# Kernel tuning notes

Measured on AMD Instinct MI355X. Metric: run time of the kernel, lower is better.

Reference implementation:

```python
import jax, jax.numpy as jnp
import numpy as np

EPS = 1e-5

def _ln(x, g, b):
    m = jnp.mean(x, axis=-1, keepdims=True)
    v = jnp.var(x, axis=-1, keepdims=True)
    return (x - m) * jax.lax.rsqrt(v + EPS) * g + b

def _gelu(x):
    return jax.nn.gelu(x, approximate=False)  # torch nn.GELU default is exact erf

def setup_inputs() -> dict:
    key = jax.random.key(0)
    B, N, D, H = 4, 1024, 128, 12
    HID = H * D
    ks = jax.random.split(key, 16)
    s = lambda k, sh, fan: jax.random.normal(k, sh, jnp.float32) * (fan ** -0.5)
    return {
        "x": jax.random.normal(ks[0], (B, N, D), jnp.float32),
        # project: LN(D) -> Linear(D,HID) -> GELU -> Linear(HID,HID)
        "ln1_g": jnp.ones((D,), jnp.float32), "ln1_b": jnp.zeros((D,), jnp.float32),
        "W1": s(ks[1], (D, HID), D), "b1": jnp.zeros((HID,), jnp.float32),
        "W2": s(ks[2], (HID, HID), HID), "b2": jnp.zeros((HID,), jnp.float32),
        # shared Attention(inc=D, outc=D)
        "aln_g": jnp.ones((D,), jnp.float32), "aln_b": jnp.zeros((D,), jnp.float32),
        "Wqkv": s(ks[3], (D, 3 * D), D), "bqkv": jnp.zeros((3 * D,), jnp.float32),
        "Wl": s(ks[4], (D, D), D), "bl": jnp.zeros((D,), jnp.float32),
        # out_proj: LN(HID) -> Linear(HID, D) -> GELU
        "lno_g": jnp.ones((HID,), jnp.float32), "lno_b": jnp.zeros((HID,), jnp.float32),
        "Wo": s(ks[5], (HID, D), HID), "bo": jnp.zeros((D,), jnp.float32),
    }

def reference(x, ln1_g, ln1_b, W1, b1, W2, b2,
              aln_g, aln_b, Wqkv, bqkv, Wl, bl,
              lno_g, lno_b, Wo, bo):
    B, N, D = x.shape
    # project (dropout is identity in eval mode)
    h = _ln(x, ln1_g, ln1_b)
    h = _gelu(h @ W1 + b1)
    h = h @ W2 + b2                      # [B, N, H*D]
    H = h.shape[-1] // D
    # chunk along last dim into H features of width D; fold heads into batch
    f = h.reshape(B, N, H, D).transpose(0, 2, 1, 3).reshape(B * H, N, D)
    # shared Attention applied to each head-chunk
    a = _ln(f, aln_g, aln_b)
    qkv = a @ Wqkv + bqkv
    q, k, v = jnp.split(qkv, 3, axis=-1)
    scores = jax.nn.softmax(jnp.einsum('bnd,bmd->bnm', q, k) * (D ** -0.5), axis=-1)
    o = jnp.einsum('bnm,bmd->bnd', scores, v)
    o = o @ Wl + bl
    o = _gelu(o + f)                     # [B*H, N, D]
    # concat heads back along last dim
    feats = o.reshape(B, H, N, D).transpose(0, 2, 1, 3).reshape(B, N, H * D)
    out = _gelu(_ln(feats, lno_g, lno_b) @ Wo + bo)
    return out
```

## Files before the change

### kernel.cpp

```cpp
#include <hip/hip_runtime.h>
#include <stdint.h>

typedef unsigned short u16;
typedef __attribute__((ext_vector_type(8))) short short8;
typedef __attribute__((ext_vector_type(4))) float floatx4;

__device__ inline float b2f(u16 u) {
  union { uint32_t i; float f; } x; x.i = ((uint32_t)u) << 16; return x.f;
}
__device__ inline u16 f2b(float f) {
  union { float f; uint32_t i; } x; x.f = f;
  uint32_t r = (x.i + 0x7FFFu + ((x.i >> 16) & 1u)) >> 16;
  return (u16)r;
}
__device__ inline float gelu_f(float v) {
  return 0.5f * v * (1.0f + erff(v * 0.70710678118654752440f));
}

#define MFMA16(a, b, c) __builtin_amdgcn_mfma_f32_16x16x32_bf16((a), (b), (c), 0, 0, 0)

__device__ __forceinline__ void gl2lds16(const u16* g, u16* l) {
  __builtin_amdgcn_global_load_lds(
      (const __attribute__((address_space(1))) uint32_t*)(uintptr_t)g,
      (__attribute__((address_space(3))) uint32_t*)(uint32_t)(uintptr_t)l,
      16, 0, 0);
}

__global__ __launch_bounds__(256)
void tpose_all_kernel(const float* __restrict__ W1, const float* __restrict__ W2,
                      const float* __restrict__ Wqkv, const float* __restrict__ Wl,
                      const float* __restrict__ Wo,
                      u16* __restrict__ w1t, u16* __restrict__ w2t,
                      u16* __restrict__ wqkvt, u16* __restrict__ wlt,
                      u16* __restrict__ wot) {
  int id = blockIdx.x;
  const float* src; u16* dst; int R, C, bx, by;
  if (id < 2304)      { src = W2;   dst = w2t;   R = 1536; C = 1536; bx = (id % 48) * 32; by = (id / 48) * 32; }
  else if (id < 2496) { id -= 2304; src = W1;   dst = w1t;   R = 128;  C = 1536; bx = (id % 48) * 32; by = (id / 48) * 32; }
  else if (id < 2688) { id -= 2496; src = Wo;   dst = wot;   R = 1536; C = 128;  bx = (id % 4) * 32;  by = (id / 4) * 32; }
  else if (id < 2736) { id -= 2688; src = Wqkv; dst = wqkvt; R = 128;  C = 384;  bx = (id % 12) * 32; by = (id / 12) * 32; }
  else                { id -= 2736; src = Wl;   dst = wlt;   R = 128;  C = 128;  bx = (id % 4) * 32;  by = (id / 4) * 32; }
  __shared__ u16 t[32][33];
  int tx = threadIdx.x & 31, ty = threadIdx.x >> 5;
  for (int i = 0; i < 32; i += 8)
    t[ty + i][tx] = f2b(src[(size_t)(by + ty + i) * C + bx + tx]);
  __syncthreads();
  for (int i = 0; i < 32; i += 8)
    dst[(size_t)(bx + ty + i) * R + by + tx] = t[tx][ty + i];
}

__global__ __launch_bounds__(256)
void ln128_f32_kernel(const float* __restrict__ X, const float* __restrict__ g,
                      const float* __restrict__ bb, u16* __restrict__ Y) {
  int tid = threadIdx.x, w = tid >> 6, lane = tid & 63;
  int row = blockIdx.x * 4 + w;
  const float* xr = X + (size_t)row * 128;
  float2 xv = *(const float2*)(xr + lane * 2);
  float x0 = xv.x, x1 = xv.y;
  float s = x0 + x1, s2 = x0 * x0 + x1 * x1;
  for (int m = 1; m < 64; m <<= 1) { s += __shfl_xor(s, m, 64); s2 += __shfl_xor(s2, m, 64); }
  float mean = s * (1.0f / 128.0f);
  float var = s2 * (1.0f / 128.0f) - mean * mean;
  float rstd = 1.0f / sqrtf(var + 1e-5f);
  float2 gv = *(const float2*)(g + lane * 2);
  float2 bv = *(const float2*)(bb + lane * 2);
  float y0 = (x0 - mean) * rstd * gv.x + bv.x;
  float y1 = (x1 - mean) * rstd * gv.y + bv.y;
  *(uint32_t*)(Y + (size_t)row * 128 + lane * 2) =
      (uint32_t)f2b(y0) | ((uint32_t)f2b(y1) << 16);
}

__global__ __launch_bounds__(256)
void ln128_perm_kernel(const u16* __restrict__ X, const float* __restrict__ g,
                       const float* __restrict__ bb, u16* __restrict__ Y) {
  int tid = threadIdx.x, w = tid >> 6, lane = tid & 63;
  int rid = blockIdx.x * 4 + w;
  int bh = rid >> 10, n = rid & 1023;
  int b = bh / 12, h = bh % 12;
  const u16* xr = X + ((size_t)(b * 1024 + n)) * 1536 + h * 128;
  uint32_t u = *(const uint32_t*)(xr + lane * 2);
  float x0 = b2f(u & 0xffff), x1 = b2f(u >> 16);
  float s = x0 + x1, s2 = x0 * x0 + x1 * x1;
  for (int m = 1; m < 64; m <<= 1) { s += __shfl_xor(s, m, 64); s2 += __shfl_xor(s2, m, 64); }
  float mean = s * (1.0f / 128.0f);
  float var = s2 * (1.0f / 128.0f) - mean * mean;
  float rstd = 1.0f / sqrtf(var + 1e-5f);
  float2 gv = *(const float2*)(g + lane * 2);
  float2 bv = *(const float2*)(bb + lane * 2);
  float y0 = (x0 - mean) * rstd * gv.x + bv.x;
  float y1 = (x1 - mean) * rstd * gv.y + bv.y;
  *(uint32_t*)(Y + (size_t)rid * 128 + lane * 2) =
      (uint32_t)f2b(y0) | ((uint32_t)f2b(y1) << 16);
}

__global__ __launch_bounds__(256)
void ln1536_kernel(const u16* __restrict__ X, const float* __restrict__ g,
                   const float* __restrict__ bb, u16* __restrict__ Y) {
  int row = blockIdx.x, tid = threadIdx.x;
  const u16* xr = X + (size_t)row * 1536;
  uint32_t u0 = *(const uint32_t*)(xr + tid * 6);
  uint32_t u1 = *(const uint32_t*)(xr + tid * 6 + 2);
  uint32_t u2 = *(const uint32_t*)(xr + tid * 6 + 4);
  float v[6] = { b2f(u0 & 0xffff), b2f(u0 >> 16), b2f(u1 & 0xffff),
                 b2f(u1 >> 16),    b2f(u2 & 0xffff), b2f(u2 >> 16) };
  float s = 0.f, s2 = 0.f;
  for (int j = 0; j < 6; j++) { s += v[j]; s2 += v[j] * v[j]; }
  for (int m = 1; m < 64; m <<= 1) { s += __shfl_xor(s, m, 64); s2 += __shfl_xor(s2, m, 64); }
  __shared__ float red[8];
  int w = tid >> 6, lane = tid & 63;
  if (lane == 0) { red[w] = s; red[4 + w] = s2; }
  __syncthreads();
  s = red[0] + red[1] + red[2] + red[3];
  s2 = red[4] + red[5] + red[6] + red[7];
  float mean = s * (1.0f / 1536.0f);
  float var = s2 * (1.0f / 1536.0f) - mean * mean;
  float rstd = 1.0f / sqrtf(var + 1e-5f);
  uint32_t o[3];
  for (int p = 0; p < 3; p++) {
    int c = tid * 6 + p * 2;
    float y0 = (v[p * 2] - mean) * rstd * g[c] + bb[c];
    float y1 = (v[p * 2 + 1] - mean) * rstd * g[c + 1] + bb[c + 1];
    o[p] = (uint32_t)f2b(y0) | ((uint32_t)f2b(y1) << 16);
  }
  u16* yr = Y + (size_t)row * 1536 + tid * 6;
  *(uint32_t*)(yr) = o[0];
  *(uint32_t*)(yr + 2) = o[1];
  *(uint32_t*)(yr + 4) = o[2];
}

__global__ __launch_bounds__(256)
void qkv_kernel(const u16* __restrict__ A, const u16* __restrict__ BT,
                const float* __restrict__ bias, u16* __restrict__ qkv,
                u16* __restrict__ vT) {
  const int K = 128;
  __shared__ __align__(16) u16 abuf[128 * 32];
  __shared__ __align__(16) u16 bbuf[128 * 32];
  int tid = threadIdx.x;
  int w = tid >> 6, lane = tid & 63, ln = lane & 15, quad = lane >> 4;
  int bm = blockIdx.x * 128, bn = blockIdx.y * 128;
  int wr = w >> 1, wc = w & 1;
  floatx4 acc[4][4] = {};
  for (int k0 = 0; k0 < K; k0 += 32) {
    __syncthreads();
    for (int rd = 0; rd < 2; rd++) {
      int c = tid + rd * 256;
      int row = c >> 2, col = (c & 3) * 8;
      gl2lds16(A + (size_t)(bm + row) * K + k0 + col, abuf + c * 8);
      gl2lds16(BT + (size_t)(bn + row) * K + k0 + col, bbuf + c * 8);
    }
    __syncthreads();
    short8 af[4], bf[4];
    for (int i = 0; i < 4; i++)
      af[i] = *(const short8*)(abuf + (wr * 64 + i * 16 + ln) * 32 + quad * 8);
    for (int j = 0; j < 4; j++)
      bf[j] = *(const short8*)(bbuf + (wc * 64 + j * 16 + ln) * 32 + quad * 8);
    for (int i = 0; i < 4; i++)
      for (int j = 0; j < 4; j++)
        acc[i][j] = MFMA16(af[i], bf[j], acc[i][j]);
  }
  if (blockIdx.y < 2) {
    const float QSCALE = 0.08838834764831845f * 1.4426950408889634f;
    float scale = (blockIdx.y == 0) ? QSCALE : 1.0f;
    for (int i = 0; i < 4; i++) {
      int row0 = bm + wr * 64 + i * 16 + quad * 4;
      for (int j = 0; j < 4; j++) {
        int col = bn + wc * 64 + j * 16 + ln;
        float bv = bias[col];
        for (int r = 0; r < 4; r++)
          qkv[(size_t)(row0 + r) * 256 + col] = f2b((acc[i][j][r] + bv) * scale);
      }
    }
  } else {
    int bh = bm >> 10;
    int nb = bm & 1023;
    u16* vp = vT + (size_t)bh * 128 * 1024;
    for (int i = 0; i < 4; i++) {
      int n0 = nb + wr * 64 + i * 16 + quad * 4;
      int npos = (n0 & ~31) | (((n0 >> 2) & 3) * 8) | (((n0 >> 4) & 1) * 4);
      for (int j = 0; j < 4; j++) {
        int d = wc * 64 + j * 16 + ln;
        float bv = bias[256 + d];
        u16 tmp[4];
        for (int r = 0; r < 4; r++) tmp[r] = f2b(acc[i][j][r] + bv);
        *(uint2*)(vp + (size_t)d * 1024 + npos) = *(const uint2*)tmp;
      }
    }
  }
}

template <int GELU, int RES, typename OUTT>
__global__ __launch_bounds__(256)
void gemm64_kernel(const u16* __restrict__ A, const u16* __restrict__ BT,
                   const float* __restrict__ bias, const u16* __restrict__ res,
                   OUTT* __restrict__ C, int M, int N, int K) {
  __shared__ __align__(16) u16 abuf[64 * 32];
  __shared__ __align__(16) u16 bbuf[128 * 32];
  int tid = threadIdx.x;
  int w = tid >> 6, lane = tid & 63, ln = lane & 15, quad = lane >> 4;
  int bm = blockIdx.x * 64, bn = blockIdx.y * 128;
  floatx4 acc[4][2] = {};
  for (int k0 = 0; k0 < K; k0 += 32) {
    __syncthreads();
    for (int rd = 0; rd < 2; rd++) {
      int c = tid + rd * 256;
      int row = c >> 2, col = (c & 3) * 8;
      gl2lds16(BT + (size_t)(bn + row) * K + k0 + col, bbuf + c * 8);
    }
    {
      int c = tid;
      int row = c >> 2, col = (c & 3) * 8;
      gl2lds16(A + (size_t)(bm + row) * K + k0 + col, abuf + c * 8);
    }
    __syncthreads();
    short8 af[4], bf[2];
    for (int i = 0; i < 4; i++)
      af[i] = *(const short8*)(abuf + (i * 16 + ln) * 32 + quad * 8);
    for (int j = 0; j < 2; j++)
      bf[j] = *(const short8*)(bbuf + (w * 32 + j * 16 + ln) * 32 + quad * 8);
    for (int i = 0; i < 4; i++)
      for (int j = 0; j < 2; j++)
        acc[i][j] = MFMA16(af[i], bf[j], acc[i][j]);
  }
  for (int i = 0; i < 4; i++) {
    int row0 = bm + i * 16 + quad * 4;
    for (int j = 0; j < 2; j++) {
      int col = bn + w * 32 + j * 16 + ln;
      float bv = bias[col];
      for (int r = 0; r < 4; r++) {
        float v = acc[i][j][r] + bv;
        if (RES) v += b2f(res[(size_t)(row0 + r) * N + col]);
        if (GELU) v = gelu_f(v);
        if constexpr (sizeof(OUTT) == 2)
          C[(size_t)(row0 + r) * N + col] = f2b(v);
        else
          C[(size_t)(row0 + r) * N + col] = v;
      }
    }
  }
}

template <int GELU, int RES, typename OUTT>
__global__ __launch_bounds__(256)
void gemm64b_kernel(const u16* __restrict__ A, const u16* __restrict__ BT,
                    const float* __restrict__ bias, const u16* __restrict__ res,
                    OUTT* __restrict__ C, int M, int N, int K) {
  __shared__ __align__(16) u16 abuf[2 * 64 * 32];
  __shared__ __align__(16) u16 bbuf[2 * 128 * 32];
  int tid = threadIdx.x;
  int w = tid >> 6, lane = tid & 63, ln = lane & 15, quad = lane >> 4;
  int bm = blockIdx.x * 64, bn = blockIdx.y * 128;
  floatx4 acc[4][2] = {};
  for (int k0 = 0; k0 < K; k0 += 64) {
    __syncthreads();
    for (int ks = 0; ks < 2; ks++) {
      {
        int c = tid;
        int row = c >> 2, cc = c & 3;
        gl2lds16(A + (size_t)(bm + row) * K + k0 + ks * 32 + cc * 8,
                 abuf + ks * 2048 + c * 8);
      }
      for (int rd = 0; rd < 2; rd++) {
        int c = tid + rd * 256;
        int row = c >> 2, cc = c & 3;
        gl2lds16(BT + (size_t)(bn + row) * K + k0 + ks * 32 + cc * 8,
                 bbuf + ks * 4096 + c * 8);
      }
    }
    __syncthreads();
    short8 af[2][4], bf[2][2];
    for (int ks = 0; ks < 2; ks++) {
      for (int i = 0; i < 4; i++)
        af[ks][i] = *(const short8*)(abuf + ks * 2048 + (i * 16 + ln) * 32 + quad * 8);
      for (int j = 0; j < 2; j++)
        bf[ks][j] = *(const short8*)(bbuf + ks * 4096 + (w * 32 + j * 16 + ln) * 32 + quad * 8);
    }
    for (int i = 0; i < 4; i++)
      for (int j = 0; j < 2; j++) {
        acc[i][j] = MFMA16(af[0][i], bf[0][j], acc[i][j]);
        acc[i][j] = MFMA16(af[1][i], bf[1][j], acc[i][j]);
      }
  }
  for (int i = 0; i < 4; i++) {
    int row0 = bm + i * 16 + quad * 4;
    for (int j = 0; j < 2; j++) {
      int col = bn + w * 32 + j * 16 + ln;
      float bv = bias[col];
      for (int r = 0; r < 4; r++) {
        float v = acc[i][j][r] + bv;
        if (RES) v += b2f(res[(size_t)(row0 + r) * N + col]);
        if (GELU) v = gelu_f(v);
        if constexpr (sizeof(OUTT) == 2)
          C[(size_t)(row0 + r) * N + col] = f2b(v);
        else
          C[(size_t)(row0 + r) * N + col] = v;
      }
    }
  }
}

__global__ __launch_bounds__(256)
void gemmwl_kernel(const u16* __restrict__ A, const u16* __restrict__ BT,
                   const float* __restrict__ bias, const u16* __restrict__ res,
                   u16* __restrict__ feats) {
  const int K = 128;
  __shared__ __align__(16) u16 abuf[64 * 32];
  __shared__ __align__(16) u16 bbuf[128 * 32];
  int tid = threadIdx.x;
  int w = tid >> 6, lane = tid & 63, ln = lane & 15, quad = lane >> 4;
  int bm = blockIdx.x * 64;
  floatx4 acc[4][2] = {};
  for (int k0 = 0; k0 < K; k0 += 32) {
    __syncthreads();
    for (int rd = 0; rd < 2; rd++) {
      int c = tid + rd * 256;
      int row = c >> 2, col = (c & 3) * 8;
      gl2lds16(BT + (size_t)row * K + k0 + col, bbuf + c * 8);
    }
    {
      int c = tid;
      int row = c >> 2, col = (c & 3) * 8;
      gl2lds16(A + (size_t)(bm + row) * K + k0 + col, abuf + c * 8);
    }
    __syncthreads();
    short8 af[4], bf[2];
    for (int i = 0; i < 4; i++)
      af[i] = *(const short8*)(abuf + (i * 16 + ln) * 32 + quad * 8);
    for (int j = 0; j < 2; j++)
      bf[j] = *(const short8*)(bbuf + (w * 32 + j * 16 + ln) * 32 + quad * 8);
    for (int i = 0; i < 4; i++)
      for (int j = 0; j < 2; j++)
        acc[i][j] = MFMA16(af[i], bf[j], acc[i][j]);
  }
  int bh = bm >> 10, nb = bm & 1023;
  int b = bh / 12, hh = bh % 12;
  size_t obase = ((size_t)b * 1024) * 1536 + hh * 128;
  for (int i = 0; i < 4; i++) {
    int n0 = nb + i * 16 + quad * 4;
    for (int j = 0; j < 2; j++) {
      int col = w * 32 + j * 16 + ln;
      float bv = bias[col];
      for (int r = 0; r < 4; r++) {
        size_t idx = obase + (size_t)(n0 + r) * 1536 + col;
        float v = acc[i][j][r] + bv + b2f(res[idx]);
        feats[idx] = f2b(gelu_f(v));
      }
    }
  }
}

__global__ __launch_bounds__(256)
void gemm64_part_kernel(const u16* __restrict__ A, const u16* __restrict__ BT,
                        float* __restrict__ pws, int Kfull, int kspan) {
  __shared__ __align__(16) u16 abuf[64 * 32];
  __shared__ __align__(16) u16 bbuf[128 * 32];
  int tid = threadIdx.x;
  int w = tid >> 6, lane = tid & 63, ln = lane & 15, quad = lane >> 4;
  int bm = blockIdx.x * 64;
  int kbeg = blockIdx.y * kspan, kend = kbeg + kspan;
  float* Cp = pws + (size_t)blockIdx.y * 4096 * 128;
  floatx4 acc[4][2] = {};
  for (int k0 = kbeg; k0 < kend; k0 += 32) {
    __syncthreads();
    for (int rd = 0; rd < 2; rd++) {
      int c = tid + rd * 256;
      int row = c >> 2, col = (c & 3) * 8;
      gl2lds16(BT + (size_t)row * Kfull + k0 + col, bbuf + c * 8);
    }
    {
      int c = tid;
      int row = c >> 2, col = (c & 3) * 8;
      gl2lds16(A + (size_t)(bm + row) * Kfull + k0 + col, abuf + c * 8);
    }
    __syncthreads();
    short8 af[4], bf[2];
    for (int i = 0; i < 4; i++)
      af[i] = *(const short8*)(abuf + (i * 16 + ln) * 32 + quad * 8);
    for (int j = 0; j < 2; j++)
      bf[j] = *(const short8*)(bbuf + (w * 32 + j * 16 + ln) * 32 + quad * 8);
    for (int i = 0; i < 4; i++)
      for (int j = 0; j < 2; j++)
        acc[i][j] = MFMA16(af[i], bf[j], acc[i][j]);
  }
  for (int i = 0; i < 4; i++) {
    int row0 = bm + i * 16 + quad * 4;
    for (int j = 0; j < 2; j++) {
      int col = w * 32 + j * 16 + ln;
      for (int r = 0; r < 4; r++)
        Cp[(size_t)(row0 + r) * 128 + col] = acc[i][j][r];
    }
  }
}

__global__ __launch_bounds__(256)
void combine_wo_kernel(const float* __restrict__ p, const float* __restrict__ bias,
                       float* __restrict__ out) {
  int i = blockIdx.x * 256 + threadIdx.x;
  const int SZ = 4096 * 128;
  float v = p[i] + p[i + SZ] + p[i + 2 * SZ] + p[i + 3 * SZ] + bias[i & 127];
  out[i] = gelu_f(v);
}

__global__ __launch_bounds__(256, 3)
void attn_kernel(const u16* __restrict__ qkv, const u16* __restrict__ vT,
                 u16* __restrict__ obuf) {
  int blk = blockIdx.x;
  int xcd = blk & 7, slot = blk >> 3;
  int bh = xcd * 6 + (slot >> 4);
  int qt = slot & 15;
  int tid = threadIdx.x, w = tid >> 6, lane = tid & 63, ln = lane & 15, quad = lane >> 4;
  int pair = w & 1, half = w >> 1;
  __shared__ __align__(16) u16 smem[24576 + 128];
  u16* kbuf = smem;
  u16* vbufs = smem + 8192;
  const int rs = 256;
  size_t base = (size_t)bh * 1024 * 256;
  const u16* qp = qkv + base;
  const u16* kp = qkv + base + 128;
  const u16* vp = vT + (size_t)bh * 128 * 1024;

  short8 qf[2][4];
  for (int g = 0; g < 2; g++) {
    int qrow = qt * 64 + pair * 32 + g * 16 + ln;
    for (int st = 0; st < 4; st++)
      qf[g][st] = *(const short8*)(qp + (size_t)qrow * rs + st * 32 + quad * 8);
  }

  short8 onesA;
  {
    short v = (ln == 0) ? (short)0x3F80 : (short)0;
    for (int j = 0; j < 8; j++) onesA[j] = v;
  }

  floatx4 o[2][8] = {};
  floatx4 l9[2] = {};

  auto STAGE_K = [&](int kt) {
    for (int it = 0; it < 4; it++) {
      int c = it * 256 + tid;
      int st = c >> 8, key = (c >> 2) & 63, cc = c & 3;
      gl2lds16(kp + (size_t)(kt * 64 + key) * rs + st * 32 + cc * 8, kbuf + c * 8);
    }
  };
  auto STAGE_V = [&](int kt, int buf) {
    u16* vb = vbufs + buf * 8192;
    for (int it = 0; it < 4; it++) {
      int c = it * 256 + tid;
      int kf = c >> 9, d = (c >> 2) & 127, cc = c & 3;
      gl2lds16(vp + (size_t)d * 1024 + kt * 64 + kf * 32 + cc * 8, vb + c * 8);
    }
  };

  STAGE_K(0);
  STAGE_V(0, 0);

  for (int kt = 0; kt < 16; kt++) {
    __syncthreads();

    short8 kfr[2][4];
    for (int tt = 0; tt < 2; tt++)
      for (int st = 0; st < 4; st++)
        kfr[tt][st] = *(const short8*)(kbuf + st * 2048 +
                                       ((half * 2 + tt) * 16 + ln) * 32 + quad * 8);
    __syncthreads();

    if (kt < 15) {
      STAGE_K(kt + 1);
      STAGE_V(kt + 1, (kt + 1) & 1);
    }

    floatx4 s[2][2] = {};
    for (int tt = 0; tt < 2; tt++)
      for (int st = 0; st < 4; st++) {
        s[0][tt] = MFMA16(kfr[tt][st], qf[0][st], s[0][tt]);
        s[1][tt] = MFMA16(kfr[tt][st], qf[1][st], s[1][tt]);
      }

    short8 pfrag[2];
    for (int g = 0; g < 2; g++) {
      float p0[4], p1[4];
      for (int r = 0; r < 4; r++) {
        p0[r] = exp2f(s[g][0][r]);
        p1[r] = exp2f(s[g][1][r]);
      }
      uint32_t a0, a1, b0, b1;
      asm("v_cvt_pk_bf16_f32 %0, %1, %2" : "=v"(a0) : "v"(p0[0]), "v"(p0[1]));
      asm("v_cvt_pk_bf16_f32 %0, %1, %2" : "=v"(a1) : "v"(p0[2]), "v"(p0[3]));
      asm("v_cvt_pk_bf16_f32 %0, %1, %2" : "=v"(b0) : "v"(p1[0]), "v"(p1[1]));
      asm("v_cvt_pk_bf16_f32 %0, %1, %2" : "=v"(b1) : "v"(p1[2]), "v"(p1[3]));
      union { uint32_t u[4]; short8 v; } pu;
      pu.u[0] = a0; pu.u[1] = a1; pu.u[2] = b0; pu.u[3] = b1;
      pfrag[g] = pu.v;
    }

    l9[0] = MFMA16(onesA, pfrag[0], l9[0]);
    l9[1] = MFMA16(onesA, pfrag[1], l9[1]);

    const u16* vb = vbufs + (kt & 1) * 8192;
    for (int dt = 0; dt < 8; dt++) {
      short8 av = *(const short8*)(vb + half * 4096 + (dt * 16 + ln) * 32 + quad * 8);
      o[0][dt] = MFMA16(av, pfrag[0], o[0][dt]);
      o[1][dt] = MFMA16(av, pfrag[1], o[1][dt]);
    }
  }

  float lsum[2];
  lsum[0] = __shfl(l9[0][0], ln);
  lsum[1] = __shfl(l9[1][0], ln);

  __syncthreads();
  float* mbuf = (float*)smem;
  float* lbuf = (float*)(smem + 16384);
  if (half == 1) {
    float* mp = mbuf + pair * 4096;
    for (int g = 0; g < 2; g++)
      for (int dt = 0; dt < 8; dt++)
        for (int r = 0; r < 4; r++)
          mp[(dt * 16 + quad * 4 + r) * 32 + ((g * 16 + ln + quad * 8) & 31)] = o[g][dt][r];
    if (quad == 0) {
      lbuf[pair * 32 + ln] = lsum[0];
      lbuf[pair * 32 + 16 + ln] = lsum[1];
    }
  }
  __syncthreads();
  if (half == 0) {
    float* mp = mbuf + pair * 4096;
    for (int g = 0; g < 2; g++) {
      float lt = lsum[g] + lbuf[pair * 32 + g * 16 + ln];
      float inv = 1.0f / lt;
      int n = qt * 64 + pair * 32 + g * 16 + ln;
      size_t ob = ((size_t)bh * 1024 + n) * 128;
      for (int dt = 0; dt < 8; dt++) {
        u16 tmp[4];
        for (int r = 0; r < 4; r++)
          tmp[r] = f2b((o[g][dt][r] +
                        mp[(dt * 16 + quad * 4 + r) * 32 + ((g * 16 + ln + quad * 8) & 31)]) * inv);
        *(uint2*)(obuf + ob + dt * 16 + quad * 4) = *(const uint2*)tmp;
      }
    }
  }
}

extern "C" void kernel_launch(void* const* d_in, const int* in_sizes, int n_in,
                              void* d_out, int out_size, void* d_ws, size_t ws_size,
                              hipStream_t stream) {
  (void)in_sizes; (void)n_in; (void)out_size; (void)ws_size;
  const float* x    = (const float*)d_in[0];
  const float* ln1g = (const float*)d_in[1];
  const float* ln1b = (const float*)d_in[2];
  const float* W1   = (const float*)d_in[3];
  const float* b1   = (const float*)d_in[4];
  const float* W2   = (const float*)d_in[5];
  const float* b2   = (const float*)d_in[6];
  const float* alng = (const float*)d_in[7];
  const float* alnb = (const float*)d_in[8];
  const float* Wqkv = (const float*)d_in[9];
  const float* bqkv = (const float*)d_in[10];
  const float* Wl   = (const float*)d_in[11];
  const float* bl   = (const float*)d_in[12];
  const float* lnog = (const float*)d_in[13];
  const float* lnob = (const float*)d_in[14];
  const float* Wo   = (const float*)d_in[15];
  const float* bo   = (const float*)d_in[16];
  float* out = (float*)d_out;

  char* ws = (char*)d_ws;
  size_t off = 0;
  auto alloc = [&](size_t elems) { u16* p = (u16*)(ws + off); off += elems * sizeof(u16); return p; };
  u16* w1t   = alloc((size_t)1536 * 128);
  u16* w2t   = alloc((size_t)1536 * 1536);
  u16* wqkvt = alloc((size_t)384 * 128);
  u16* wlt   = alloc((size_t)128 * 128);
  u16* wot   = alloc((size_t)128 * 1536);
  u16* lnx   = alloc((size_t)4096 * 128);
  u16* h1    = alloc((size_t)4096 * 1536);
  u16* h2    = alloc((size_t)4096 * 1536);
  u16* aln   = alloc((size_t)49152 * 128);
  u16* qkv   = alloc((size_t)49152 * 256);
  u16* obuf  = alloc((size_t)49152 * 128);
  u16* vT = h1;
  u16* feats = aln;
  u16* lnf = qkv;
  float* pws = (float*)h1;

  dim3 T(256);
  tpose_all_kernel<<<dim3(2752), T, 0, stream>>>(W1, W2, Wqkv, Wl, Wo,
                                                 w1t, w2t, wqkvt, wlt, wot);
  ln128_f32_kernel<<<dim3(4096 / 4), T, 0, stream>>>(x, ln1g, ln1b, lnx);
  gemm64_kernel<1, 0, u16><<<dim3(4096 / 64, 1536 / 128), T, 0, stream>>>(
      lnx, w1t, b1, nullptr, h1, 4096, 1536, 128);
  gemm64b_kernel<0, 0, u16><<<dim3(4096 / 64, 1536 / 128), T, 0, stream>>>(
      h1, w2t, b2, nullptr, h2, 4096, 1536, 1536);
  ln128_perm_kernel<<<dim3(49152 / 4), T, 0, stream>>>(h2, alng, alnb, aln);
  qkv_kernel<<<dim3(49152 / 128, 3), T, 0, stream>>>(aln, wqkvt, bqkv, qkv, vT);
  attn_kernel<<<dim3(768), T, 0, stream>>>(qkv, vT, obuf);
  gemmwl_kernel<<<dim3(49152 / 64), T, 0, stream>>>(obuf, wlt, bl, h2, feats);
  ln1536_kernel<<<dim3(4096), T, 0, stream>>>(feats, lnog, lnob, lnf);
  gemm64_part_kernel<<<dim3(4096 / 64, 4), T, 0, stream>>>(lnf, wot, pws, 1536, 384);
  combine_wo_kernel<<<dim3(4096 * 128 / 256), T, 0, stream>>>(pws, bo, out);
}
```

Before: 248.0 us.

## Double-buffer LDS tiles in GEMM kernels to overlap loads with MFMA

Four GEMM kernels (qkv, gemm64, gemm64b, gemm64_part) get doubled LDS buffers. Each iteration now prefetches the next K-slab with async global-to-LDS loads while the current slab feeds the MFMAs. This hides global load latency behind compute and drops one barrier per iteration. The cost is twice the LDS per block, which may lower occupancy. Short K loops, such as K=128 in the qkv kernel, get little overlap.

```diff
diff --git a/kernel.cpp b/kernel.cpp
--- a/kernel.cpp
+++ b/kernel.cpp
@@ -133,27 +133,35 @@
                 const float* __restrict__ bias, u16* __restrict__ qkv,
                 u16* __restrict__ vT) {
   const int K = 128;
-  __shared__ __align__(16) u16 abuf[128 * 32];
-  __shared__ __align__(16) u16 bbuf[128 * 32];
+  __shared__ __align__(16) u16 abuf[2 * 128 * 32];
+  __shared__ __align__(16) u16 bbuf[2 * 128 * 32];
   int tid = threadIdx.x;
   int w = tid >> 6, lane = tid & 63, ln = lane & 15, quad = lane >> 4;
   int bm = blockIdx.x * 128, bn = blockIdx.y * 128;
   int wr = w >> 1, wc = w & 1;
   floatx4 acc[4][4] = {};
-  for (int k0 = 0; k0 < K; k0 += 32) {
-    __syncthreads();
+  auto STAGE = [&](int k0, int buf) {
+    u16* ab = abuf + buf * 4096;
+    u16* bb = bbuf + buf * 4096;
     for (int rd = 0; rd < 2; rd++) {
       int c = tid + rd * 256;
       int row = c >> 2, col = (c & 3) * 8;
-      gl2lds16(A + (size_t)(bm + row) * K + k0 + col, abuf + c * 8);
-      gl2lds16(BT + (size_t)(bn + row) * K + k0 + col, bbuf + c * 8);
-    }
-    __syncthreads();
+      gl2lds16(A + (size_t)(bm + row) * K + k0 + col, ab + c * 8);
+      gl2lds16(BT + (size_t)(bn + row) * K + k0 + col, bb + c * 8);
+    }
+  };
+  STAGE(0, 0);
+  int it = 0;
+  for (int k0 = 0; k0 < K; k0 += 32, it++) {
+    __syncthreads();
+    if (k0 + 32 < K) STAGE(k0 + 32, (it + 1) & 1);
+    const u16* ab = abuf + (it & 1) * 4096;
+    const u16* bb = bbuf + (it & 1) * 4096;
     short8 af[4], bf[4];
     for (int i = 0; i < 4; i++)
-      af[i] = *(const short8*)(abuf + (wr * 64 + i * 16 + ln) * 32 + quad * 8);
+      af[i] = *(const short8*)(ab + (wr * 64 + i * 16 + ln) * 32 + quad * 8);
     for (int j = 0; j < 4; j++)
-      bf[j] = *(const short8*)(bbuf + (wc * 64 + j * 16 + ln) * 32 + quad * 8);
+      bf[j] = *(const short8*)(bb + (wc * 64 + j * 16 + ln) * 32 + quad * 8);
     for (int i = 0; i < 4; i++)
       for (int j = 0; j < 4; j++)
         acc[i][j] = MFMA16(af[i], bf[j], acc[i][j]);
@@ -193,30 +201,38 @@
 void gemm64_kernel(const u16* __restrict__ A, const u16* __restrict__ BT,
                    const float* __restrict__ bias, const u16* __restrict__ res,
                    OUTT* __restrict__ C, int M, int N, int K) {
-  __shared__ __align__(16) u16 abuf[64 * 32];
-  __shared__ __align__(16) u16 bbuf[128 * 32];
+  __shared__ __align__(16) u16 abuf[2 * 64 * 32];
+  __shared__ __align__(16) u16 bbuf[2 * 128 * 32];
   int tid = threadIdx.x;
   int w = tid >> 6, lane = tid & 63, ln = lane & 15, quad = lane >> 4;
   int bm = blockIdx.x * 64, bn = blockIdx.y * 128;
   floatx4 acc[4][2] = {};
-  for (int k0 = 0; k0 < K; k0 += 32) {
-    __syncthreads();
+  auto STAGE = [&](int k0, int buf) {
+    u16* ab = abuf + buf * 2048;
+    u16* bb = bbuf + buf * 4096;
     for (int rd = 0; rd < 2; rd++) {
       int c = tid + rd * 256;
       int row = c >> 2, col = (c & 3) * 8;
-      gl2lds16(BT + (size_t)(bn + row) * K + k0 + col, bbuf + c * 8);
+      gl2lds16(BT + (size_t)(bn + row) * K + k0 + col, bb + c * 8);
     }
     {
       int c = tid;
       int row = c >> 2, col = (c & 3) * 8;
-      gl2lds16(A + (size_t)(bm + row) * K + k0 + col, abuf + c * 8);
-    }
-    __syncthreads();
+      gl2lds16(A + (size_t)(bm + row) * K + k0 + col, ab + c * 8);
+    }
+  };
+  STAGE(0, 0);
+  int it = 0;
+  for (int k0 = 0; k0 < K; k0 += 32, it++) {
+    __syncthreads();
+    if (k0 + 32 < K) STAGE(k0 + 32, (it + 1) & 1);
+    const u16* ab = abuf + (it & 1) * 2048;
+    const u16* bb = bbuf + (it & 1) * 4096;
     short8 af[4], bf[2];
     for (int i = 0; i < 4; i++)
-      af[i] = *(const short8*)(abuf + (i * 16 + ln) * 32 + quad * 8);
+      af[i] = *(const short8*)(ab + (i * 16 + ln) * 32 + quad * 8);
     for (int j = 0; j < 2; j++)
-      bf[j] = *(const short8*)(bbuf + (w * 32 + j * 16 + ln) * 32 + quad * 8);
+      bf[j] = *(const short8*)(bb + (w * 32 + j * 16 + ln) * 32 + quad * 8);
     for (int i = 0; i < 4; i++)
       for (int j = 0; j < 2; j++)
         acc[i][j] = MFMA16(af[i], bf[j], acc[i][j]);
@@ -244,35 +260,43 @@
 void gemm64b_kernel(const u16* __restrict__ A, const u16* __restrict__ BT,
                     const float* __restrict__ bias, const u16* __restrict__ res,
                     OUTT* __restrict__ C, int M, int N, int K) {
-  __shared__ __align__(16) u16 abuf[2 * 64 * 32];
-  __shared__ __align__(16) u16 bbuf[2 * 128 * 32];
+  __shared__ __align__(16) u16 abuf[2 * 2 * 64 * 32];
+  __shared__ __align__(16) u16 bbuf[2 * 2 * 128 * 32];
   int tid = threadIdx.x;
   int w = tid >> 6, lane = tid & 63, ln = lane & 15, quad = lane >> 4;
   int bm = blockIdx.x * 64, bn = blockIdx.y * 128;
   floatx4 acc[4][2] = {};
-  for (int k0 = 0; k0 < K; k0 += 64) {
-    __syncthreads();
+  auto STAGE = [&](int k0, int buf) {
+    u16* ab = abuf + buf * 4096;
+    u16* bb = bbuf + buf * 8192;
     for (int ks = 0; ks < 2; ks++) {
       {
         int c = tid;
         int row = c >> 2, cc = c & 3;
         gl2lds16(A + (size_t)(bm + row) * K + k0 + ks * 32 + cc * 8,
-                 abuf + ks * 2048 + c * 8);
+                 ab + ks * 2048 + c * 8);
       }
       for (int rd = 0; rd < 2; rd++) {
         int c = tid + rd * 256;
         int row = c >> 2, cc = c & 3;
         gl2lds16(BT + (size_t)(bn + row) * K + k0 + ks * 32 + cc * 8,
-                 bbuf + ks * 4096 + c * 8);
-      }
-    }
-    __syncthreads();
+                 bb + ks * 4096 + c * 8);
+      }
+    }
+  };
+  STAGE(0, 0);
+  int it = 0;
+  for (int k0 = 0; k0 < K; k0 += 64, it++) {
+    __syncthreads();
+    if (k0 + 64 < K) STAGE(k0 + 64, (it + 1) & 1);
+    const u16* ab = abuf + (it & 1) * 4096;
+    const u16* bb = bbuf + (it & 1) * 8192;
     short8 af[2][4], bf[2][2];
     for (int ks = 0; ks < 2; ks++) {
       for (int i = 0; i < 4; i++)
-        af[ks][i] = *(const short8*)(abuf + ks * 2048 + (i * 16 + ln) * 32 + quad * 8);
+        af[ks][i] = *(const short8*)(ab + ks * 2048 + (i * 16 + ln) * 32 + quad * 8);
       for (int j = 0; j < 2; j++)
-        bf[ks][j] = *(const short8*)(bbuf + ks * 4096 + (w * 32 + j * 16 + ln) * 32 + quad * 8);
+        bf[ks][j] = *(const short8*)(bb + ks * 4096 + (w * 32 + j * 16 + ln) * 32 + quad * 8);
     }
     for (int i = 0; i < 4; i++)
       for (int j = 0; j < 2; j++) {
@@ -351,32 +375,40 @@
 __global__ __launch_bounds__(256)
 void gemm64_part_kernel(const u16* __restrict__ A, const u16* __restrict__ BT,
                         float* __restrict__ pws, int Kfull, int kspan) {
-  __shared__ __align__(16) u16 abuf[64 * 32];
-  __shared__ __align__(16) u16 bbuf[128 * 32];
+  __shared__ __align__(16) u16 abuf[2 * 64 * 32];
+  __shared__ __align__(16) u16 bbuf[2 * 128 * 32];
   int tid = threadIdx.x;
   int w = tid >> 6, lane = tid & 63, ln = lane & 15, quad = lane >> 4;
   int bm = blockIdx.x * 64;
   int kbeg = blockIdx.y * kspan, kend = kbeg + kspan;
   float* Cp = pws + (size_t)blockIdx.y * 4096 * 128;
   floatx4 acc[4][2] = {};
-  for (int k0 = kbeg; k0 < kend; k0 += 32) {
-    __syncthreads();
+  auto STAGE = [&](int k0, int buf) {
+    u16* ab = abuf + buf * 2048;
+    u16* bb = bbuf + buf * 4096;
     for (int rd = 0; rd < 2; rd++) {
       int c = tid + rd * 256;
       int row = c >> 2, col = (c & 3) * 8;
-      gl2lds16(BT + (size_t)row * Kfull + k0 + col, bbuf + c * 8);
+      gl2lds16(BT + (size_t)row * Kfull + k0 + col, bb + c * 8);
     }
     {
       int c = tid;
       int row = c >> 2, col = (c & 3) * 8;
-      gl2lds16(A + (size_t)(bm + row) * Kfull + k0 + col, abuf + c * 8);
-    }
-    __syncthreads();
+      gl2lds16(A + (size_t)(bm + row) * Kfull + k0 + col, ab + c * 8);
+    }
+  };
+  STAGE(kbeg, 0);
+  int it = 0;
+  for (int k0 = kbeg; k0 < kend; k0 += 32, it++) {
+    __syncthreads();
+    if (k0 + 32 < kend) STAGE(k0 + 32, (it + 1) & 1);
+    const u16* ab = abuf + (it & 1) * 2048;
+    const u16* bb = bbuf + (it & 1) * 4096;
     short8 af[4], bf[2];
     for (int i = 0; i < 4; i++)
-      af[i] = *(const short8*)(abuf + (i * 16 + ln) * 32 + quad * 8);
+      af[i] = *(const short8*)(ab + (i * 16 + ln) * 32 + quad * 8);
     for (int j = 0; j < 2; j++)
-      bf[j] = *(const short8*)(bbuf + (w * 32 + j * 16 + ln) * 32 + quad * 8);
+      bf[j] = *(const short8*)(bb + (w * 32 + j * 16 + ln) * 32 + quad * 8);
     for (int i = 0; i < 4; i++)
       for (int j = 0; j < 2; j++)
         acc[i][j] = MFMA16(af[i], bf[j], acc[i][j]);
```

New measurement: 239.8 us. -3.3%, faster.
